# Kernel optimization log

Measured on AMD Instinct MI355X. Metric: run time of the kernel, lower is better.

## Reference

```python
import jax, jax.numpy as jnp
import numpy as np

N_USER = 20000
N_ITEM = 20000
N = N_USER + N_ITEM          # total nodes
D = 128                      # n_hid (= in_feats = out_feats)
H = 4                        # GAT heads
L = 2                        # n_layers
M = 8                        # mem_size (hypernet bottleneck)
T = 5                        # num_rels in MemoryLayer
E_UI = 40000                 # user->item bipartite edges
E_T = 16000                  # homogeneous edges per relation type (grouped)
EPS = 1e-5


def _layer_norm(x, w, b):
    mu = x.mean(-1, keepdims=True)
    var = ((x - mu) ** 2).mean(-1, keepdims=True)
    return (x - mu) * jax.lax.rsqrt(var + EPS) * w + b


def _gat(h_src, h_dst, src_idx, dst_idx, n_dst, W, al, ar, bias):
    """DGL GATConv (shared fc, eval-mode dropout=identity, elu activation)."""
    fs = (h_src @ W.T).reshape(-1, H, D)          # [Ns, H, D]
    fd = (h_dst @ W.T).reshape(-1, H, D)          # [Nd, H, D]
    el = (fs * al).sum(-1)                        # [Ns, H]
    er = (fd * ar).sum(-1)                        # [Nd, H]
    e = jax.nn.leaky_relu(el[src_idx] + er[dst_idx], 0.2)   # [E, H]
    emax = jax.ops.segment_max(e, dst_idx, num_segments=n_dst)
    ex = jnp.exp(e - emax[dst_idx])
    denom = jax.ops.segment_sum(ex, dst_idx, num_segments=n_dst)
    a = ex / denom[dst_idx]                       # edge softmax per dst
    rst = jax.ops.segment_sum(a[:, :, None] * fs[src_idx], dst_idx, num_segments=n_dst)
    return jax.nn.elu(rst + bias.reshape(1, H, D))           # [Nd, H, D]


def _memory_layer(feat, edge_src, edge_dst, Wc, bc, Ww, nWc, nbc, nWw, h_bias, ln_w, ln_b):
    # edges grouped by relation type: edge_src/edge_dst are [T, E_T]
    hs = feat[edge_src]                           # [T, Et, D]
    hd = feat[edge_dst]                           # [T, Et, D]
    # per-edge hypernetwork: coef = LeakyReLU(Linear(dst)); w = Ww(coef); msg = w @ src
    coef = jax.nn.leaky_relu(jnp.einsum('ted,tmd->tem', hd, Wc) + bc[:, None, :], 0.2)
    tmp = jnp.einsum('tei,tmoi->temo', hs, Ww)    # [T, Et, M, D] -- M-bottleneck path
    msg = jnp.einsum('tem,temo->teo', coef, tmp)  # [T, Et, D]
    flat_dst = edge_dst.reshape(-1)
    s = jax.ops.segment_sum(msg.reshape(-1, D), flat_dst, num_segments=N)
    cnt = jax.ops.segment_sum(jnp.ones((flat_dst.shape[0],), feat.dtype), flat_dst, num_segments=N)
    agg = s / jnp.maximum(cnt, 1.0)[:, None]      # fn.mean (0 for isolated nodes)
    rep = _layer_norm(agg, ln_w, ln_b) + h_bias
    # self-loop node_ME(feat, feat)
    ncoef = jax.nn.leaky_relu(feat @ nWc.T + nbc, 0.2)       # [N, M]
    ntmp = jnp.einsum('ni,moi->nmo', feat, nWw)              # [N, M, D]
    rep = rep + jnp.einsum('nm,nmo->no', ncoef, ntmp)
    return jax.nn.leaky_relu(rep, 0.2)            # dropout = identity (eval)


def setup_inputs() -> dict:
    key = jax.random.key(0)
    ks = jax.random.split(key, 16)
    s = 0.05
    return {
        "embedding": jax.random.normal(ks[0], (N, D), jnp.float32),
        "gat_fc_W": jax.random.normal(ks[1], (L, 2, H * D, D), jnp.float32) * s,
        "gat_attn_l": jax.random.normal(ks[2], (L, 2, H, D), jnp.float32) * s,
        "gat_attn_r": jax.random.normal(ks[3], (L, 2, H, D), jnp.float32) * s,
        "gat_bias": jnp.zeros((L, 2, H * D), jnp.float32),
        "proj_W": jax.random.normal(ks[4], (L, 2, D, H * D), jnp.float32) * s,
        "proj_b": jnp.zeros((L, 2, D), jnp.float32),
        "mem_rel_Wc": jax.random.normal(ks[5], (L, T, M, D), jnp.float32) * s,
        "mem_rel_bc": jnp.zeros((L, T, M), jnp.float32),
        "mem_rel_Ww": jax.random.normal(ks[6], (L, T, M, D, D), jnp.float32) * s,
        "mem_node_Wc": jax.random.normal(ks[7], (L, M, D), jnp.float32) * s,
        "mem_node_bc": jnp.zeros((L, M), jnp.float32),
        "mem_node_Ww": jax.random.normal(ks[8], (L, M, D, D), jnp.float32) * s,
        "mem_h_bias": jnp.zeros((L, D), jnp.float32),
        "mem_ln_w": jnp.ones((L, D), jnp.float32),
        "mem_ln_b": jnp.zeros((L, D), jnp.float32),
        "final_ln_w": jnp.ones(((L + 1) * D,), jnp.float32),
        "final_ln_b": jnp.zeros(((L + 1) * D,), jnp.float32),
        "src_u": jax.random.randint(ks[9], (E_UI,), 0, N_USER, jnp.int32),
        "dst_i": jax.random.randint(ks[10], (E_UI,), 0, N_ITEM, jnp.int32),
        "edge_src": jax.random.randint(ks[11], (T, E_T), 0, N, jnp.int32),
        "edge_dst": jax.random.randint(ks[12], (T, E_T), 0, N, jnp.int32),
    }


def reference(embedding, gat_fc_W, gat_attn_l, gat_attn_r, gat_bias, proj_W, proj_b,
              mem_rel_Wc, mem_rel_bc, mem_rel_Ww, mem_node_Wc, mem_node_bc, mem_node_Ww,
              mem_h_bias, mem_ln_w, mem_ln_b, final_ln_w, final_ln_b,
              src_u, dst_i, edge_src, edge_dst):
    features = embedding
    all_emb = [features]
    for l in range(L):
        hu, hi = features[:N_USER], features[N_USER:]
        # relation 0: item -> user (dst = user)
        gu = _gat(hi, hu, dst_i, src_u, N_USER,
                  gat_fc_W[l, 0], gat_attn_l[l, 0], gat_attn_r[l, 0], gat_bias[l, 0])
        ru = jax.nn.elu(gu.reshape(N_USER, H * D) @ proj_W[l, 0].T + proj_b[l, 0])
        # relation 1: user -> item (dst = item)
        gi = _gat(hu, hi, src_u, dst_i, N_ITEM,
                  gat_fc_W[l, 1], gat_attn_l[l, 1], gat_attn_r[l, 1], gat_bias[l, 1])
        ri = jnp.asarray(jax.nn.elu(gi.reshape(N_ITEM, H * D) @ proj_W[l, 1].T + proj_b[l, 1]))
        trans = jnp.concatenate([ru, ri], axis=0)             # [N, D]
        mem = _memory_layer(all_emb[-1], edge_src, edge_dst,
                            mem_rel_Wc[l], mem_rel_bc[l], mem_rel_Ww[l],
                            mem_node_Wc[l], mem_node_bc[l], mem_node_Ww[l],
                            mem_h_bias[l], mem_ln_w[l], mem_ln_b[l])
        features = mem + trans
        all_emb.append(features)
    return _layer_norm(jnp.concatenate(all_emb, axis=1), final_ln_w, final_ln_b)
```

## Files before the change

### kernel.cpp

```cpp
#include <hip/hip_runtime.h>
#include <hip/hip_bf16.h>
#include <math.h>

typedef __hip_bfloat16 bf16;

#define NUSER 20000
#define NITEM 20000
#define NTOT  40000
#define DD    128
#define HH    4
#define TT    5
#define MMEM  8
#define EUI   40000
#define ET    16000

#define MP_N  40064
#define MP_H  20096

typedef __attribute__((ext_vector_type(8))) short short8;
typedef __attribute__((ext_vector_type(4))) float f32x4;

__device__ __forceinline__ void gload16(const bf16* g, bf16* l){
  __builtin_amdgcn_global_load_lds(
      (const __attribute__((address_space(1))) unsigned int*)g,
      (__attribute__((address_space(3))) unsigned int*)l, 16, 0, 0);
}
__device__ __forceinline__ float bu2f_lo(unsigned u){ return __uint_as_float(u << 16); }
__device__ __forceinline__ float bu2f_hi(unsigned u){ return __uint_as_float(u & 0xffff0000u); }

__device__ __forceinline__ int stage_cg(int lane){
  return (((lane&3) ^ ((lane>>2)&3) ^ (lane>>4)) << 3);
}
__device__ __forceinline__ int read_pc8(int lm, int lq){
  return ((lq ^ (lm&3) ^ ((lm>>2)&3)) << 3);
}

__global__ __launch_bounds__(256) void k_mfma_gemm(
    const bf16* __restrict__ A, const bf16* __restrict__ B,
    const float* __restrict__ bias, float* __restrict__ C,
    long Astr, long Bstr, long biasStr, long Cstr,
    int ldc, int M, int K, int act, int accum)
{
  A += (size_t)blockIdx.z*Astr; B += (size_t)blockIdx.z*Bstr;
  if (bias) bias += (size_t)blockIdx.z*biasStr;
  C += (size_t)blockIdx.z*Cstr;
  __shared__ bf16 As[128*32];
  __shared__ bf16 Bs[128*32];
  int tid = threadIdx.x;
  int wave = tid >> 6, lane = tid & 63;
  int r0 = blockIdx.x * 128, c0 = blockIdx.y * 128;
  int wm = (wave >> 1) * 64, wn = (wave & 1) * 64;
  f32x4 acc[4][4];
  #pragma unroll
  for (int i=0;i<4;i++)
    #pragma unroll
    for (int j=0;j<4;j++) acc[i][j] = (f32x4){0.f,0.f,0.f,0.f};

  int rq = lane >> 2;
  int cg = stage_cg(lane);
  const bf16* Ag = A + (size_t)(r0 + wave*32 + rq)*K + cg;
  const bf16* Bg = B + (size_t)(c0 + wave*32 + rq)*K + cg;
  bf16* AsW = As + wave*32*32;
  bf16* BsW = Bs + wave*32*32;
  int lm = lane & 15, lq = lane >> 4;
  int pc8 = read_pc8(lm, lq);
  const bf16* Ard = As + (wm + lm)*32 + pc8;
  const bf16* Brd = Bs + (wn + lm)*32 + pc8;

  for (int k0 = 0; k0 < K; k0 += 32){
    gload16(Ag + k0,            AsW);
    gload16(Ag + 16*K + k0,     AsW + 16*32);
    gload16(Bg + k0,            BsW);
    gload16(Bg + 16*K + k0,     BsW + 16*32);
    __syncthreads();
    short8 af[4], bfv[4];
    #pragma unroll
    for (int i=0;i<4;i++) af[i]  = *(const short8*)(Ard + i*16*32);
    #pragma unroll
    for (int j=0;j<4;j++) bfv[j] = *(const short8*)(Brd + j*16*32);
    #pragma unroll
    for (int i=0;i<4;i++)
      #pragma unroll
      for (int j=0;j<4;j++)
        acc[i][j] = __builtin_amdgcn_mfma_f32_16x16x32_bf16(af[i], bfv[j], acc[i][j], 0, 0, 0);
    __syncthreads();
  }
  #pragma unroll
  for (int i=0;i<4;i++){
    #pragma unroll
    for (int j=0;j<4;j++){
      int c = c0 + wn + j*16 + lm;
      #pragma unroll
      for (int rg=0; rg<4; rg++){
        int r = r0 + wm + i*16 + lq*4 + rg;
        if (r < M){
          float v = acc[i][j][rg];
          if (bias) v += bias[c];
          if (act==1) v = v>0.f ? v : expm1f(v);
          float* cp = &C[(size_t)r*ldc + c];
          if (accum) *cp += v; else *cp = v;
        }
      }
    }
  }
}

__global__ __launch_bounds__(256) void k_fc_gemm(
    const bf16* __restrict__ A, const bf16* __restrict__ B,
    bf16* __restrict__ Fb, const float* __restrict__ al, const float* __restrict__ ar,
    float* __restrict__ el, float* __restrict__ er, int M)
{
  __shared__ bf16 As[128*32];
  __shared__ bf16 Bs[128*32];
  __shared__ float redE[2][2][128];
  int tid = threadIdx.x;
  int wave = tid >> 6, lane = tid & 63;
  int h = blockIdx.y;
  int r0 = blockIdx.x * 128;
  int wm = (wave >> 1) * 64, wn = (wave & 1) * 64;
  f32x4 acc[4][4];
  #pragma unroll
  for (int i=0;i<4;i++)
    #pragma unroll
    for (int j=0;j<4;j++) acc[i][j] = (f32x4){0.f,0.f,0.f,0.f};

  int rq = lane >> 2;
  int cg = stage_cg(lane);
  const bf16* Ag = A + (size_t)(r0 + wave*32 + rq)*128 + cg;
  const bf16* Bg = B + (size_t)(h*128 + wave*32 + rq)*128 + cg;
  bf16* AsW = As + wave*32*32;
  bf16* BsW = Bs + wave*32*32;
  int lm = lane & 15, lq = lane >> 4;
  int pc8 = read_pc8(lm, lq);
  const bf16* Ard = As + (wm + lm)*32 + pc8;
  const bf16* Brd = Bs + (wn + lm)*32 + pc8;

  for (int k0 = 0; k0 < 128; k0 += 32){
    gload16(Ag + k0,             AsW);
    gload16(Ag + 16*128 + k0,    AsW + 16*32);
    gload16(Bg + k0,             BsW);
    gload16(Bg + 16*128 + k0,    BsW + 16*32);
    __syncthreads();
    short8 af[4], bfv[4];
    #pragma unroll
    for (int i=0;i<4;i++) af[i]  = *(const short8*)(Ard + i*16*32);
    #pragma unroll
    for (int j=0;j<4;j++) bfv[j] = *(const short8*)(Brd + j*16*32);
    #pragma unroll
    for (int i=0;i<4;i++)
      #pragma unroll
      for (int j=0;j<4;j++)
        acc[i][j] = __builtin_amdgcn_mfma_f32_16x16x32_bf16(af[i], bfv[j], acc[i][j], 0, 0, 0);
    __syncthreads();
  }
  float alv[4], arv[4];
  #pragma unroll
  for (int j=0;j<4;j++){
    int c = h*128 + wn + j*16 + lm;
    alv[j] = al[c]; arv[j] = ar[c];
  }
  int wnh = wave & 1;
  #pragma unroll
  for (int i=0;i<4;i++){
    #pragma unroll
    for (int rg=0; rg<4; rg++){
      float se = 0.f, sr = 0.f;
      #pragma unroll
      for (int j=0;j<4;j++){
        float v = acc[i][j][rg];
        se = fmaf(v, alv[j], se);
        sr = fmaf(v, arv[j], sr);
      }
      #pragma unroll
      for (int msk=1; msk<16; msk<<=1){
        se += __shfl_xor(se, msk);
        sr += __shfl_xor(sr, msk);
      }
      if (lm == 0){
        int rl = wm + i*16 + lq*4 + rg;
        redE[0][wnh][rl] = se;
        redE[1][wnh][rl] = sr;
      }
    }
  }
  #pragma unroll
  for (int i=0;i<4;i++){
    #pragma unroll
    for (int j=0;j<4;j++){
      int c = h*128 + wn + j*16 + lm;
      #pragma unroll
      for (int rg=0; rg<4; rg++){
        int r = r0 + wm + i*16 + lq*4 + rg;
        if (r < M) Fb[(size_t)r*512 + c] = __float2bfloat16(acc[i][j][rg]);
      }
    }
  }
  __syncthreads();
  if (tid < 128){
    int r = r0 + tid;
    if (r < M) el[(size_t)r*4 + h] = redE[0][0][tid] + redE[0][1][tid];
  } else {
    int t2 = tid - 128;
    int r = r0 + t2;
    if (r < M) er[(size_t)r*4 + h] = redE[1][0][t2] + redE[1][1][t2];
  }
}

__global__ __launch_bounds__(256) void k_memgemm(
    const float* __restrict__ feat, const int* __restrict__ src,
    const float* __restrict__ coef, const bf16* __restrict__ B,
    float* __restrict__ C, bf16* __restrict__ Cb,
    const float* __restrict__ trans, float* __restrict__ fout,
    long srcStr, long coefStr, long Bstr, long CbStr,
    int Mvalid, int mode)
{
  __shared__ bf16 Af[64*136];
  __shared__ float cfS[8*64];
  int t = blockIdx.y;
  const int*   srcT  = src ? src + (size_t)t*srcStr : nullptr;
  const float* coefT = coef + (size_t)t*coefStr;
  const bf16*  Bt    = B + (size_t)t*Bstr;
  int tid = threadIdx.x, wave = tid >> 6, lane = tid & 63;
  int r0 = blockIdx.x * 64;

  {
    int rL = tid >> 2, seg = tid & 3;
    int r = r0 + rL;
    bool valid = r < Mvalid;
    int s = valid ? (srcT ? srcT[r] : r) : 0;
    const float4* fp = (const float4*)(feat + (size_t)s*128 + seg*32);
    bf16* ap = Af + rL*136 + seg*32;
    #pragma unroll
    for (int q=0;q<8;q+=2){
      float4 v0 = fp[q], v1 = fp[q+1];
      *(__hip_bfloat162*)(ap + q*4)     = __float22bfloat162_rn(make_float2(v0.x, v0.y));
      *(__hip_bfloat162*)(ap + q*4 + 2) = __float22bfloat162_rn(make_float2(v0.z, v0.w));
      *(__hip_bfloat162*)(ap + q*4 + 4) = __float22bfloat162_rn(make_float2(v1.x, v1.y));
      *(__hip_bfloat162*)(ap + q*4 + 6) = __float22bfloat162_rn(make_float2(v1.z, v1.w));
    }
  }
  if (tid < 64){
    int r = r0 + tid;
    bool valid = r < Mvalid;
    #pragma unroll
    for (int m=0;m<8;m++)
      cfS[m*64 + tid] = valid ? coefT[(size_t)r*8 + m] : 0.f;
  }
  __syncthreads();

  int wm = (wave >> 1) * 32, wn = (wave & 1) * 64;
  int lm = lane & 15, lq = lane >> 4;

  short8 afr[4][2];
  #pragma unroll
  for (int ic=0; ic<4; ic++)
    #pragma unroll
    for (int i=0; i<2; i++)
      afr[ic][i] = *(const short8*)(Af + (size_t)(wm + i*16 + lm)*136 + ic*32 + lq*8);

  const bf16* Bl0 = Bt + (size_t)(wn +  0 + lm)*1024 + lq*8;
  const bf16* Bl1 = Bt + (size_t)(wn + 16 + lm)*1024 + lq*8;
  const bf16* Bl2 = Bt + (size_t)(wn + 32 + lm)*1024 + lq*8;
  const bf16* Bl3 = Bt + (size_t)(wn + 48 + lm)*1024 + lq*8;

  f32x4 accC[2][4];
  #pragma unroll
  for (int i=0;i<2;i++)
    #pragma unroll
    for (int j=0;j<4;j++) accC[i][j] = (f32x4){0.f,0.f,0.f,0.f};

  #pragma unroll
  for (int m = 0; m < 8; m++){
    f32x4 accM[2][4];
    #pragma unroll
    for (int ic = 0; ic < 4; ic++){
      int ko = m*128 + ic*32;
      short8 bfv[4];
      bfv[0] = *(const short8*)(Bl0 + ko);
      bfv[1] = *(const short8*)(Bl1 + ko);
      bfv[2] = *(const short8*)(Bl2 + ko);
      bfv[3] = *(const short8*)(Bl3 + ko);
      if (ic == 0){
        #pragma unroll
        for (int i=0;i<2;i++)
          #pragma unroll
          for (int j=0;j<4;j++)
            accM[i][j] = __builtin_amdgcn_mfma_f32_16x16x32_bf16(afr[ic][i], bfv[j],
                             (f32x4){0.f,0.f,0.f,0.f}, 0, 0, 0);
      } else {
        #pragma unroll
        for (int i=0;i<2;i++)
          #pragma unroll
          for (int j=0;j<4;j++)
            accM[i][j] = __builtin_amdgcn_mfma_f32_16x16x32_bf16(afr[ic][i], bfv[j], accM[i][j], 0, 0, 0);
      }
    }
    #pragma unroll
    for (int i=0;i<2;i++){
      f32x4 cf4 = *(const f32x4*)(cfS + m*64 + wm + i*16 + lq*4);
      #pragma unroll
      for (int j=0;j<4;j++)
        #pragma unroll
        for (int rg=0; rg<4; rg++)
          accC[i][j][rg] = fmaf(cf4[rg], accM[i][j][rg], accC[i][j][rg]);
    }
  }

  #pragma unroll
  for (int i=0;i<2;i++){
    #pragma unroll
    for (int j=0;j<4;j++){
      int c = wn + j*16 + lm;
      #pragma unroll
      for (int rg=0; rg<4; rg++){
        int r = r0 + wm + i*16 + lq*4 + rg;
        if (r < Mvalid){
          float v = accC[i][j][rg];
          if (mode == 0){
            Cb[(size_t)t*CbStr + (size_t)r*128 + c] = __float2bfloat16(v);
          } else {
            float x = C[(size_t)r*128 + c] + v;
            x = x>0.f ? x : 0.2f*x;
            fout[(size_t)r*128 + c] = x + trans[(size_t)r*128 + c];
          }
        }
      }
    }
  }
}

__global__ void k_f2b(const float* __restrict__ in, bf16* __restrict__ o, int nv, int nt){
  int i = blockIdx.x*256 + threadIdx.x;
  if (i < nt) o[i] = __float2bfloat16(i < nv ? in[i] : 0.f);
}

__global__ void k_repack(const float* __restrict__ in, bf16* __restrict__ o){
  int s = blockIdx.y;
  int g = blockIdx.x*256 + threadIdx.x;
  int m = g >> 14, od = (g >> 7) & 127, i = g & 127;
  o[(size_t)s*131072 + (size_t)od*1024 + m*128 + i] = __float2bfloat16(in[(size_t)s*131072 + g]);
}

__global__ void k_hist(const int* __restrict__ dIdx, int* __restrict__ cnt, int E){
  int e = blockIdx.x*256+threadIdx.x;
  if (e<E) atomicAdd(&cnt[dIdx[e]], 1);
}

__global__ __launch_bounds__(1024) void k_scan(const int* __restrict__ in,
                                               int* __restrict__ out, int n){
  __shared__ int wsum[16];
  __shared__ int carry;
  int tidx = threadIdx.x, lane = tidx & 63, w = tidx >> 6;
  if (tidx == 0) carry = 0;
  __syncthreads();
  for (int base = 0; base < n; base += 1024){
    int i = base + tidx;
    int v = (i < n) ? in[i] : 0;
    int x = v;
    #pragma unroll
    for (int off = 1; off < 64; off <<= 1){
      int t = __shfl_up(x, off);
      if (lane >= off) x += t;
    }
    if (lane == 63) wsum[w] = x;
    __syncthreads();
    if (w == 0 && lane < 16){
      int t = wsum[lane];
      #pragma unroll
      for (int off=1; off<16; off<<=1){
        int u = __shfl_up(t, off, 16);
        if (lane >= off) t += u;
      }
      wsum[lane] = t;
    }
    __syncthreads();
    int woff = (w == 0) ? 0 : wsum[w-1];
    int excl = carry + woff + x - v;
    if (i < n) out[i] = excl;
    __syncthreads();
    if (tidx == 1023) carry = carry + wsum[15];
    __syncthreads();
  }
  if (tidx == 0) out[n] = carry;
}

__global__ void k_csr_scatter(const int* __restrict__ sIdx, const int* __restrict__ dIdx,
                              int sOff, const int* __restrict__ rowptr,
                              int* __restrict__ cursor, int* __restrict__ col, int E){
  int e = blockIdx.x*256+threadIdx.x; if (e>=E) return;
  int d = dIdx[e];
  int pos = rowptr[d] + atomicAdd(&cursor[d], 1);
  col[pos] = sIdx[e] + sOff;
}

__global__ void k_csr_scatter_eid(const int* __restrict__ dIdx, const int* __restrict__ rowptr,
                                  int* __restrict__ cursor, int* __restrict__ col, int E){
  int e = blockIdx.x*256+threadIdx.x; if (e>=E) return;
  int d = dIdx[e];
  int pos = rowptr[d] + atomicAdd(&cursor[d], 1);
  col[pos] = e;
}

__global__ __launch_bounds__(64) void k_gat_gather(
    const int* __restrict__ rowptr, const int* __restrict__ col,
    const float* __restrict__ el, const float* __restrict__ er,
    const bf16* __restrict__ Fb, const float* __restrict__ gb,
    bf16* __restrict__ rstb, int dOff)
{
  int dl = blockIdx.x;
  int lane = threadIdx.x;
  int h = lane >> 4;
  int off = (lane & 15) << 3;
  float erh = er[(size_t)(dl + dOff)*4 + h];
  float m = -INFINITY, den = 0.f;
  float acc[8];
  #pragma unroll
  for (int i=0;i<8;i++) acc[i]=0.f;
  int jb = rowptr[dl], je = rowptr[dl+1];
  for (int j=jb; j<je; j++){
    int s = col[j];
    float e = el[(size_t)s*4+h] + erh;
    e = e > 0.f ? e : 0.2f*e;
    float mn = fmaxf(m, e);
    float sc = __expf(m - mn);
    float wj = __expf(e - mn);
    den = den*sc + wj;
    m = mn;
    uint4 u = *(const uint4*)(Fb + (size_t)s*512 + h*128 + off);
    acc[0]=acc[0]*sc + wj*bu2f_lo(u.x); acc[1]=acc[1]*sc + wj*bu2f_hi(u.x);
    acc[2]=acc[2]*sc + wj*bu2f_lo(u.y); acc[3]=acc[3]*sc + wj*bu2f_hi(u.y);
    acc[4]=acc[4]*sc + wj*bu2f_lo(u.z); acc[5]=acc[5]*sc + wj*bu2f_hi(u.z);
    acc[6]=acc[6]*sc + wj*bu2f_lo(u.w); acc[7]=acc[7]*sc + wj*bu2f_hi(u.w);
  }
  float inv = den > 0.f ? 1.f/den : 0.f;
  int cb = h*128 + off;
  float x[8];
  #pragma unroll
  for (int q=0;q<8;q++){
    float v = acc[q]*inv + gb[cb+q];
    x[q] = v>0.f ? v : expm1f(v);
  }
  union { uint4 u; __hip_bfloat162 p[4]; } O;
  #pragma unroll
  for (int q=0;q<4;q++) O.p[q] = __float22bfloat162_rn(make_float2(x[2*q], x[2*q+1]));
  *(uint4*)(rstb + (size_t)dl*512 + cb) = O.u;
}

__global__ void k_coef(const float* __restrict__ feat, const int* __restrict__ idx,
                       const float* __restrict__ Wc, const float* __restrict__ bc,
                       float* __restrict__ outc, int cnt){
  int t = blockIdx.y;
  __shared__ float wT[DD*MMEM];
  __shared__ float bS[MMEM];
  for (int i=threadIdx.x;i<MMEM*DD;i+=128){
    int m = i >> 7, d = i & 127;
    wT[d*MMEM + m] = Wc[(size_t)t*MMEM*DD + i];
  }
  if (threadIdx.x < MMEM) bS[threadIdx.x] = bc[t*MMEM + threadIdx.x];
  __syncthreads();
  int e = blockIdx.x*128 + threadIdx.x; if (e >= cnt) return;
  int node = idx ? idx[(size_t)t*cnt + e] : e;
  float acc[MMEM];
  #pragma unroll
  for (int m=0;m<MMEM;m++) acc[m]=bS[m];
  const float4* fr = (const float4*)(feat + (size_t)node*DD);
  for (int d4=0; d4<32; d4++){
    float4 v = fr[d4];
    const float* w0 = wT + d4*4*MMEM;
    #pragma unroll
    for (int m=0;m<MMEM;m++) acc[m] = fmaf(v.x, w0[m], acc[m]);
    #pragma unroll
    for (int m=0;m<MMEM;m++) acc[m] = fmaf(v.y, w0[MMEM+m], acc[m]);
    #pragma unroll
    for (int m=0;m<MMEM;m++) acc[m] = fmaf(v.z, w0[2*MMEM+m], acc[m]);
    #pragma unroll
    for (int m=0;m<MMEM;m++) acc[m] = fmaf(v.w, w0[3*MMEM+m], acc[m]);
  }
  float* op = outc + ((size_t)t*cnt + e)*MMEM;
  #pragma unroll
  for (int m=0;m<MMEM;m++){ float v=acc[m]; op[m] = v>0.f ? v : 0.2f*v; }
}

__global__ void k_mem_gather(const int* __restrict__ rpT, const int* __restrict__ colT,
                             const bf16* __restrict__ msg, float* __restrict__ sAgg){
  int n = blockIdx.x*4 + (threadIdx.x >> 6);
  if (n >= NTOT) return;
  int lane = threadIdx.x & 63;
  int jb = rpT[n], je = rpT[n+1];
  float a0=0.f, a1=0.f;
  for (int j=jb;j<je;j++){
    unsigned u = ((const unsigned*)(msg + (size_t)colT[j]*128))[lane];
    a0 += bu2f_lo(u); a1 += bu2f_hi(u);
  }
  *(float2*)(sAgg + (size_t)n*128 + lane*2) = make_float2(a0, a1);
}

__global__ void k_memln(const float* __restrict__ s, const int* __restrict__ rpT,
                        const float* __restrict__ lw, const float* __restrict__ lb,
                        const float* __restrict__ hb, float* __restrict__ outp){
  int n = blockIdx.x, lane = threadIdx.x;
  float c = fmaxf((float)(rpT[n+1]-rpT[n]), 1.f);
  float x1 = s[(size_t)n*128+lane]/c, x2 = s[(size_t)n*128+64+lane]/c;
  float t = x1+x2;
  #pragma unroll
  for (int off=32;off;off>>=1) t += __shfl_xor(t,off);
  float mu = t * (1.f/128.f);
  float d1=x1-mu, d2=x2-mu;
  float v = d1*d1+d2*d2;
  #pragma unroll
  for (int off=32;off;off>>=1) v += __shfl_xor(v,off);
  float r = rsqrtf(v*(1.f/128.f) + 1e-5f);
  outp[(size_t)n*128+lane]    = d1*r*lw[lane]    + lb[lane]    + hb[lane];
  outp[(size_t)n*128+64+lane] = d2*r*lw[64+lane] + lb[64+lane] + hb[64+lane];
}

__global__ void k_final_ln(const float* __restrict__ emb, const float* __restrict__ f1,
                           const float* __restrict__ f2, const float* __restrict__ w,
                           const float* __restrict__ b, float* __restrict__ out){
  int n = blockIdx.x, t = threadIdx.x;
  __shared__ float red[4];
  float x0 = emb[(size_t)n*128+t];
  float x1 = f1[(size_t)n*128+t];
  float x2 = f2[(size_t)n*128+t];
  float s = x0+x1+x2;
  #pragma unroll
  for (int off=32;off;off>>=1) s += __shfl_xor(s,off);
  if ((t&63)==0) red[t>>6] = s;
  __syncthreads();
  float mu = (red[0]+red[1]) * (1.f/384.f);
  float d0=x0-mu, d1=x1-mu, d2=x2-mu;
  float v = d0*d0+d1*d1+d2*d2;
  #pragma unroll
  for (int off=32;off;off>>=1) v += __shfl_xor(v,off);
  if ((t&63)==0) red[2+(t>>6)] = v;
  __syncthreads();
  float var = (red[2]+red[3]) * (1.f/384.f);
  float r = rsqrtf(var + 1e-5f);
  size_t o = (size_t)n*384;
  out[o+t]     = d0*r*w[t]     + b[t];
  out[o+128+t] = d1*r*w[128+t] + b[128+t];
  out[o+256+t] = d2*r*w[256+t] + b[256+t];
}

extern "C" void kernel_launch(void* const* d_in, const int* in_sizes, int n_in,
                              void* d_out, int out_size, void* d_ws, size_t ws_size,
                              hipStream_t stream)
{
  const float* emb   = (const float*)d_in[0];
  const float* fcW   = (const float*)d_in[1];
  const float* attl  = (const float*)d_in[2];
  const float* attr  = (const float*)d_in[3];
  const float* gbias = (const float*)d_in[4];
  const float* projW = (const float*)d_in[5];
  const float* projB = (const float*)d_in[6];
  const float* relWc = (const float*)d_in[7];
  const float* relbc = (const float*)d_in[8];
  const float* relWw = (const float*)d_in[9];
  const float* nodWc = (const float*)d_in[10];
  const float* nodbc = (const float*)d_in[11];
  const float* nodWw = (const float*)d_in[12];
  const float* hbias = (const float*)d_in[13];
  const float* mlnw  = (const float*)d_in[14];
  const float* mlnb  = (const float*)d_in[15];
  const float* flnw  = (const float*)d_in[16];
  const float* flnb  = (const float*)d_in[17];
  const int*  srcU  = (const int*)d_in[18];
  const int*  dstI  = (const int*)d_in[19];
  const int*  eSrc  = (const int*)d_in[20];
  const int*  eDst  = (const int*)d_in[21];
  float* out = (float*)d_out;

  char* wp = (char*)d_ws;
  auto alloc = [&](size_t bytes)->void* {
    void* p = (void*)wp; wp += (bytes + 511) & ~(size_t)511; return p;
  };
  float* feat1 = (float*)alloc((size_t)NTOT*DD*4);
  float* feat2 = (float*)alloc((size_t)NTOT*DD*4);
  float* Fbuf  = (float*)alloc((size_t)NTOT*512*4);
  float* rst   = (float*)alloc((size_t)NTOT*DD*2*4);
  bf16*  rstb0 = (bf16*)alloc((size_t)2*MP_H*512*2);
  float* trans = (float*)alloc((size_t)NTOT*DD*4);
  float* elF   = (float*)alloc((size_t)NTOT*4*4);
  float* erF   = (float*)alloc((size_t)NTOT*4*4);
  int* rpA  = (int*)alloc((size_t)(NUSER+1)*4);
  int* colA = (int*)alloc((size_t)EUI*4);
  int* rpB  = (int*)alloc((size_t)(NITEM+1)*4);
  int* colB = (int*)alloc((size_t)EUI*4);
  int* icnt = (int*)alloc((size_t)20000*4);
  int* icur = (int*)alloc((size_t)20000*4);
  int* rpT  = (int*)alloc((size_t)(NTOT+1)*4);
  int* colT = (int*)alloc((size_t)TT*ET*4);
  int* cntT = (int*)alloc((size_t)NTOT*4);
  int* icurT= (int*)alloc((size_t)NTOT*4);
  bf16* featb  = (bf16*)alloc((size_t)MP_N*DD*2);
  bf16* fcWb   = (bf16*)alloc((size_t)4*512*DD*2);
  bf16* projWb = (bf16*)alloc((size_t)4*DD*512*2);
  bf16* relWwb = (bf16*)alloc((size_t)10*DD*1024*2);
  bf16* nodWwb = (bf16*)alloc((size_t)2*DD*1024*2);
  bf16*  Fb     = (bf16*)Fbuf;
  bf16*  msgBb  = (bf16*)((char*)Fbuf + (size_t)NTOT*512*2);
  float* coefB  = (float*)((char*)msgBb + (size_t)TT*ET*128*2);
  float* ncoefB = coefB + (size_t)TT*ET*8;
  bf16*  rstb1  = rstb0 + (size_t)MP_H*512;
  float* sAgg   = rst;
  float* memO   = rst + (size_t)NTOT*DD;

  k_f2b<<<dim3((4*512*DD+255)/256),256,0,stream>>>(fcW, fcWb, 4*512*DD, 4*512*DD);
  k_f2b<<<dim3((4*DD*512+255)/256),256,0,stream>>>(projW, projWb, 4*DD*512, 4*DD*512);
  k_repack<<<dim3(512,10),256,0,stream>>>(relWw, relWwb);
  k_repack<<<dim3(512,2),256,0,stream>>>(nodWw, nodWwb);
  hipMemsetAsync(rstb0 + (size_t)20000*512, 0, (size_t)(MP_H-20000)*512*2, stream);
  hipMemsetAsync(rstb1 + (size_t)20000*512, 0, (size_t)(MP_H-20000)*512*2, stream);

  hipMemsetAsync(icnt, 0, 20000*4, stream);
  hipMemsetAsync(icur, 0, 20000*4, stream);
  k_hist<<<dim3((EUI+255)/256),256,0,stream>>>(srcU, icnt, EUI);
  k_scan<<<dim3(1),1024,0,stream>>>(icnt, rpA, NUSER);
  k_csr_scatter<<<dim3((EUI+255)/256),256,0,stream>>>(dstI, srcU, NUSER, rpA, icur, colA, EUI);
  hipMemsetAsync(icnt, 0, 20000*4, stream);
  hipMemsetAsync(icur, 0, 20000*4, stream);
  k_hist<<<dim3((EUI+255)/256),256,0,stream>>>(dstI, icnt, EUI);
  k_scan<<<dim3(1),1024,0,stream>>>(icnt, rpB, NITEM);
  k_csr_scatter<<<dim3((EUI+255)/256),256,0,stream>>>(srcU, dstI, 0, rpB, icur, colB, EUI);
  hipMemsetAsync(cntT, 0, NTOT*4, stream);
  hipMemsetAsync(icurT, 0, NTOT*4, stream);
  k_hist<<<dim3((TT*ET+255)/256),256,0,stream>>>(eDst, cntT, TT*ET);
  k_scan<<<dim3(1),1024,0,stream>>>(cntT, rpT, NTOT);
  k_csr_scatter_eid<<<dim3((TT*ET+255)/256),256,0,stream>>>(eDst, rpT, icurT, colT, TT*ET);

  const float* feats[3] = {emb, feat1, feat2};
  for (int l=0; l<2; l++){
    const float* fin  = feats[l];
    float* fout = (float*)feats[l+1];

    k_f2b<<<dim3((MP_N*DD+255)/256),256,0,stream>>>(fin, featb, NTOT*DD, MP_N*DD);

    for (int d=0; d<2; d++){
      k_fc_gemm<<<dim3(MP_N/128, 4),256,0,stream>>>(
          featb, fcWb + (size_t)(l*2+d)*512*DD, Fb,
          attl+(size_t)(l*2+d)*512, attr+(size_t)(l*2+d)*512, elF, erF, NTOT);
      int dOff = (d==0) ? 0 : NUSER;
      const int* rp  = (d==0) ? rpA : rpB;
      const int* col = (d==0) ? colA : colB;
      k_gat_gather<<<dim3(20000),64,0,stream>>>(rp, col, elF, erF, Fb,
          gbias+(size_t)(l*2+d)*512, (d==0) ? rstb0 : rstb1, dOff);
    }
    k_mfma_gemm<<<dim3(MP_H/128, 1, 2),256,0,stream>>>(
        rstb0, projWb + (size_t)(l*2)*DD*512, projB + (size_t)(l*2)*DD, trans,
        (long)MP_H*512, (long)DD*512, (long)DD, (long)20000*DD,
        DD, 20000, 512, 1, 0);

    k_coef<<<dim3((ET+127)/128, TT),128,0,stream>>>(fin, eDst,
        relWc+(size_t)l*TT*MMEM*DD, relbc+(size_t)l*TT*MMEM, coefB, ET);
    k_memgemm<<<dim3(ET/64, TT),256,0,stream>>>(
        fin, eSrc, coefB, relWwb + (size_t)l*TT*DD*1024,
        nullptr, msgBb, nullptr, nullptr,
        (long)ET, (long)ET*8, (long)DD*1024, (long)ET*128, ET, 0);
    k_mem_gather<<<dim3(NTOT/4),256,0,stream>>>(rpT, colT, msgBb, sAgg);
    k_memln<<<dim3(NTOT),64,0,stream>>>(sAgg, rpT, mlnw+(size_t)l*DD, mlnb+(size_t)l*DD,
                                        hbias+(size_t)l*DD, memO);
    k_coef<<<dim3((NTOT+127)/128, 1),128,0,stream>>>(fin, nullptr,
        nodWc+(size_t)l*MMEM*DD, nodbc+(size_t)l*MMEM, ncoefB, NTOT);
    k_memgemm<<<dim3(MP_N/64, 1),256,0,stream>>>(
        fin, nullptr, ncoefB, nodWwb + (size_t)l*DD*1024,
        memO, nullptr, trans, fout,
        0, 0, 0, 0, NTOT, 2);
  }

  k_final_ln<<<dim3(NTOT),128,0,stream>>>(emb, feat1, feat2, flnw, flnb, out);
}
```

Before: 1.021 ms.

## Retile memgemm B weights into k-chunks and double-buffer B loads

Repacks the hypernetwork weight matrix so that each 32-wide k-chunk for all 128 output columns is contiguous, which gives compact, coalesced B fragment loads. The memgemm inner loop now prefetches the next chunk's B fragments into a second register set while the MFMAs for the current chunk run. It also adds a minimum occupancy of 3 blocks per CU to launch_bounds. The aim is to hide global load latency for B. The extra register buffer, combined with the occupancy target, could lead to spills.

New measurement: 1.805 ms. 1.77x slower.

```diff
diff --git a/kernel.cpp b/kernel.cpp
--- a/kernel.cpp
+++ b/kernel.cpp
@@ -206,7 +206,7 @@
   }
 }
 
-__global__ __launch_bounds__(256) void k_memgemm(
+__global__ __launch_bounds__(256,3) void k_memgemm(
     const float* __restrict__ feat, const int* __restrict__ src,
     const float* __restrict__ coef, const bf16* __restrict__ B,
     float* __restrict__ C, bf16* __restrict__ Cb,
@@ -258,10 +258,33 @@
     for (int i=0; i<2; i++)
       afr[ic][i] = *(const short8*)(Af + (size_t)(wm + i*16 + lm)*136 + ic*32 + lq*8);
 
-  const bf16* Bl0 = Bt + (size_t)(wn +  0 + lm)*1024 + lq*8;
-  const bf16* Bl1 = Bt + (size_t)(wn + 16 + lm)*1024 + lq*8;
-  const bf16* Bl2 = Bt + (size_t)(wn + 32 + lm)*1024 + lq*8;
-  const bf16* Bl3 = Bt + (size_t)(wn + 48 + lm)*1024 + lq*8;
+  const bf16* Bl = Bt + (size_t)(wn + lm)*32 + lq*8;
+
+#define LDB(dst, kc) do{                                    \
+    const bf16* _p = Bl + (size_t)(kc)*4096;                \
+    dst[0] = *(const short8*)(_p);                          \
+    dst[1] = *(const short8*)(_p + 512);                    \
+    dst[2] = *(const short8*)(_p + 1024);                   \
+    dst[3] = *(const short8*)(_p + 1536);                   \
+  }while(0)
+
+#define MFMA_STEP(ic, bv) do{                                                        \
+    if ((ic)==0){                                                                    \
+      _Pragma("unroll")                                                              \
+      for (int i=0;i<2;i++)                                                          \
+        _Pragma("unroll")                                                            \
+        for (int j=0;j<4;j++)                                                        \
+          accM[i][j] = __builtin_amdgcn_mfma_f32_16x16x32_bf16(afr[0][i], bv[j],     \
+                           (f32x4){0.f,0.f,0.f,0.f}, 0, 0, 0);                       \
+    } else {                                                                         \
+      _Pragma("unroll")                                                              \
+      for (int i=0;i<2;i++)                                                          \
+        _Pragma("unroll")                                                            \
+        for (int j=0;j<4;j++)                                                        \
+          accM[i][j] = __builtin_amdgcn_mfma_f32_16x16x32_bf16(afr[ic][i], bv[j],    \
+                           accM[i][j], 0, 0, 0);                                     \
+    }                                                                                \
+  }while(0)
 
   f32x4 accC[2][4];
   #pragma unroll
@@ -269,30 +292,21 @@
     #pragma unroll
     for (int j=0;j<4;j++) accC[i][j] = (f32x4){0.f,0.f,0.f,0.f};
 
+  short8 bcur[4], bnxt[4];
+  LDB(bcur, 0);
+  f32x4 accM[2][4];
+
   #pragma unroll
   for (int m = 0; m < 8; m++){
-    f32x4 accM[2][4];
     #pragma unroll
     for (int ic = 0; ic < 4; ic++){
-      int ko = m*128 + ic*32;
-      short8 bfv[4];
-      bfv[0] = *(const short8*)(Bl0 + ko);
-      bfv[1] = *(const short8*)(Bl1 + ko);
-      bfv[2] = *(const short8*)(Bl2 + ko);
-      bfv[3] = *(const short8*)(Bl3 + ko);
-      if (ic == 0){
-        #pragma unroll
-        for (int i=0;i<2;i++)
-          #pragma unroll
-          for (int j=0;j<4;j++)
-            accM[i][j] = __builtin_amdgcn_mfma_f32_16x16x32_bf16(afr[ic][i], bfv[j],
-                             (f32x4){0.f,0.f,0.f,0.f}, 0, 0, 0);
+      const int kc = m*4 + ic;
+      if ((kc & 1) == 0){
+        if (kc + 1 < 32) LDB(bnxt, kc+1);
+        MFMA_STEP(ic, bcur);
       } else {
-        #pragma unroll
-        for (int i=0;i<2;i++)
-          #pragma unroll
-          for (int j=0;j<4;j++)
-            accM[i][j] = __builtin_amdgcn_mfma_f32_16x16x32_bf16(afr[ic][i], bfv[j], accM[i][j], 0, 0, 0);
+        if (kc + 1 < 32) LDB(bcur, kc+1);
+        MFMA_STEP(ic, bnxt);
       }
     }
     #pragma unroll
@@ -305,6 +319,8 @@
           accC[i][j][rg] = fmaf(cf4[rg], accM[i][j][rg], accC[i][j][rg]);
     }
   }
+#undef LDB
+#undef MFMA_STEP
 
   #pragma unroll
   for (int i=0;i<2;i++){
@@ -338,7 +354,9 @@
   int s = blockIdx.y;
   int g = blockIdx.x*256 + threadIdx.x;
   int m = g >> 14, od = (g >> 7) & 127, i = g & 127;
-  o[(size_t)s*131072 + (size_t)od*1024 + m*128 + i] = __float2bfloat16(in[(size_t)s*131072 + g]);
+  int k = m*128 + i;
+  int kc = k >> 5, ki = k & 31;
+  o[(size_t)s*131072 + ((size_t)kc*128 + od)*32 + ki] = __float2bfloat16(in[(size_t)s*131072 + g]);
 }
 
 __global__ void k_hist(const int* __restrict__ dIdx, int* __restrict__ cnt, int E){
```

## Fold hypernet coefficients into a K=1024 A matrix and reuse the generic MFMA GEMM

Applied to the files above, without the earlier changes.

Replaces the fused memory-layer kernel, which ran eight K=128 MFMA passes per tile and scaled each by per-row coefficients, with two steps. A new kernel first writes a bf16 A matrix of coef[m]*feat rows (K=1024), and the shared LDS-staged MFMA GEMM then multiplies it by the repacked Ww weights. The GEMM epilogue gains bf16 output and a fused leaky-relu plus trans-add mode. This aims for a better-pipelined, LDS-tiled GEMM at the cost of materialising a large intermediate (about 165MB for the relation path), plus a fallback that runs per relation or per half when the workspace is too small.

Result: slower. 1.338 ms (+31.0%).

```diff
diff --git a/kernel.cpp b/kernel.cpp
--- a/kernel.cpp
+++ b/kernel.cpp
@@ -16,6 +16,7 @@
 
 #define MP_N  40064
 #define MP_H  20096
+#define EP_PAD 16128
 
 typedef __attribute__((ext_vector_type(8))) short short8;
 typedef __attribute__((ext_vector_type(4))) float f32x4;
@@ -37,13 +38,14 @@
 
 __global__ __launch_bounds__(256) void k_mfma_gemm(
     const bf16* __restrict__ A, const bf16* __restrict__ B,
-    const float* __restrict__ bias, float* __restrict__ C,
-    long Astr, long Bstr, long biasStr, long Cstr,
-    int ldc, int M, int K, int act, int accum)
+    const float* __restrict__ bias,
+    float* __restrict__ C, bf16* __restrict__ Cb,
+    const float* __restrict__ Cin, const float* __restrict__ trans,
+    long Astr, long Bstr, long biasStr, long Cstr, long CbStr,
+    int ldc, int M, int K, int act)
 {
   A += (size_t)blockIdx.z*Astr; B += (size_t)blockIdx.z*Bstr;
   if (bias) bias += (size_t)blockIdx.z*biasStr;
-  C += (size_t)blockIdx.z*Cstr;
   __shared__ bf16 As[128*32];
   __shared__ bf16 Bs[128*32];
   int tid = threadIdx.x;
@@ -97,8 +99,13 @@
           float v = acc[i][j][rg];
           if (bias) v += bias[c];
           if (act==1) v = v>0.f ? v : expm1f(v);
-          float* cp = &C[(size_t)r*ldc + c];
-          if (accum) *cp += v; else *cp = v;
+          if (act==2){
+            float x = Cin[(size_t)r*128 + c] + v;
+            x = x>0.f ? x : 0.2f*x;
+            v = x + trans[(size_t)r*128 + c];
+          }
+          if (Cb) Cb[(size_t)blockIdx.z*CbStr + (size_t)r*ldc + c] = __float2bfloat16(v);
+          else    C [(size_t)blockIdx.z*Cstr  + (size_t)r*ldc + c] = v;
         }
       }
     }
@@ -206,127 +213,31 @@
   }
 }
 
-__global__ __launch_bounds__(256) void k_memgemm(
-    const float* __restrict__ feat, const int* __restrict__ src,
-    const float* __restrict__ coef, const bf16* __restrict__ B,
-    float* __restrict__ C, bf16* __restrict__ Cb,
-    const float* __restrict__ trans, float* __restrict__ fout,
-    long srcStr, long coefStr, long Bstr, long CbStr,
-    int Mvalid, int mode)
+__global__ void k_bldA(const float* __restrict__ feat, const int* __restrict__ src,
+                       const float* __restrict__ cf, bf16* __restrict__ out,
+                       int rows, int rowsPad, int rowOff,
+                       long srcStr, long cfStr, long outStr)
 {
-  __shared__ bf16 Af[64*136];
-  __shared__ float cfS[8*64];
   int t = blockIdx.y;
-  const int*   srcT  = src ? src + (size_t)t*srcStr : nullptr;
-  const float* coefT = coef + (size_t)t*coefStr;
-  const bf16*  Bt    = B + (size_t)t*Bstr;
-  int tid = threadIdx.x, wave = tid >> 6, lane = tid & 63;
-  int r0 = blockIdx.x * 64;
-
-  {
-    int rL = tid >> 2, seg = tid & 3;
-    int r = r0 + rL;
-    bool valid = r < Mvalid;
-    int s = valid ? (srcT ? srcT[r] : r) : 0;
-    const float4* fp = (const float4*)(feat + (size_t)s*128 + seg*32);
-    bf16* ap = Af + rL*136 + seg*32;
-    #pragma unroll
-    for (int q=0;q<8;q+=2){
-      float4 v0 = fp[q], v1 = fp[q+1];
-      *(__hip_bfloat162*)(ap + q*4)     = __float22bfloat162_rn(make_float2(v0.x, v0.y));
-      *(__hip_bfloat162*)(ap + q*4 + 2) = __float22bfloat162_rn(make_float2(v0.z, v0.w));
-      *(__hip_bfloat162*)(ap + q*4 + 4) = __float22bfloat162_rn(make_float2(v1.x, v1.y));
-      *(__hip_bfloat162*)(ap + q*4 + 6) = __float22bfloat162_rn(make_float2(v1.z, v1.w));
-    }
-  }
-  if (tid < 64){
-    int r = r0 + tid;
-    bool valid = r < Mvalid;
-    #pragma unroll
-    for (int m=0;m<8;m++)
-      cfS[m*64 + tid] = valid ? coefT[(size_t)r*8 + m] : 0.f;
-  }
-  __syncthreads();
-
-  int wm = (wave >> 1) * 32, wn = (wave & 1) * 64;
-  int lm = lane & 15, lq = lane >> 4;
-
-  short8 afr[4][2];
-  #pragma unroll
-  for (int ic=0; ic<4; ic++)
-    #pragma unroll
-    for (int i=0; i<2; i++)
-      afr[ic][i] = *(const short8*)(Af + (size_t)(wm + i*16 + lm)*136 + ic*32 + lq*8);
-
-  const bf16* Bl0 = Bt + (size_t)(wn +  0 + lm)*1024 + lq*8;
-  const bf16* Bl1 = Bt + (size_t)(wn + 16 + lm)*1024 + lq*8;
-  const bf16* Bl2 = Bt + (size_t)(wn + 32 + lm)*1024 + lq*8;
-  const bf16* Bl3 = Bt + (size_t)(wn + 48 + lm)*1024 + lq*8;
-
-  f32x4 accC[2][4];
-  #pragma unroll
-  for (int i=0;i<2;i++)
-    #pragma unroll
-    for (int j=0;j<4;j++) accC[i][j] = (f32x4){0.f,0.f,0.f,0.f};
-
-  #pragma unroll
-  for (int m = 0; m < 8; m++){
-    f32x4 accM[2][4];
-    #pragma unroll
-    for (int ic = 0; ic < 4; ic++){
-      int ko = m*128 + ic*32;
-      short8 bfv[4];
-      bfv[0] = *(const short8*)(Bl0 + ko);
-      bfv[1] = *(const short8*)(Bl1 + ko);
-      bfv[2] = *(const short8*)(Bl2 + ko);
-      bfv[3] = *(const short8*)(Bl3 + ko);
-      if (ic == 0){
-        #pragma unroll
-        for (int i=0;i<2;i++)
-          #pragma unroll
-          for (int j=0;j<4;j++)
-            accM[i][j] = __builtin_amdgcn_mfma_f32_16x16x32_bf16(afr[ic][i], bfv[j],
-                             (f32x4){0.f,0.f,0.f,0.f}, 0, 0, 0);
-      } else {
-        #pragma unroll
-        for (int i=0;i<2;i++)
-          #pragma unroll
-          for (int j=0;j<4;j++)
-            accM[i][j] = __builtin_amdgcn_mfma_f32_16x16x32_bf16(afr[ic][i], bfv[j], accM[i][j], 0, 0, 0);
-      }
-    }
-    #pragma unroll
-    for (int i=0;i<2;i++){
-      f32x4 cf4 = *(const f32x4*)(cfS + m*64 + wm + i*16 + lq*4);
-      #pragma unroll
-      for (int j=0;j<4;j++)
-        #pragma unroll
-        for (int rg=0; rg<4; rg++)
-          accC[i][j][rg] = fmaf(cf4[rg], accM[i][j][rg], accC[i][j][rg]);
-    }
-  }
-
-  #pragma unroll
-  for (int i=0;i<2;i++){
-    #pragma unroll
-    for (int j=0;j<4;j++){
-      int c = wn + j*16 + lm;
-      #pragma unroll
-      for (int rg=0; rg<4; rg++){
-        int r = r0 + wm + i*16 + lq*4 + rg;
-        if (r < Mvalid){
-          float v = accC[i][j][rg];
-          if (mode == 0){
-            Cb[(size_t)t*CbStr + (size_t)r*128 + c] = __float2bfloat16(v);
-          } else {
-            float x = C[(size_t)r*128 + c] + v;
-            x = x>0.f ? x : 0.2f*x;
-            fout[(size_t)r*128 + c] = x + trans[(size_t)r*128 + c];
-          }
-        }
-      }
-    }
-  }
+  long g = (long)blockIdx.x*256 + threadIdx.x;
+  long row = g >> 7;
+  if (row >= rowsPad) return;
+  int grp = (int)(g & 127);
+  int k0 = grp*8, m = k0 >> 7, i0 = k0 & 127;
+  bool valid = row < rows;
+  int s = 0; float c = 0.f;
+  if (valid){
+    s = src ? src[(size_t)t*srcStr + row] : (int)(rowOff + row);
+    c = cf[((size_t)t*cfStr + rowOff + row)*8 + m];
+  }
+  const float4* fp = (const float4*)(feat + (size_t)s*128 + i0);
+  float4 v0 = fp[0], v1 = fp[1];
+  union { uint4 u; __hip_bfloat162 p[4]; } O;
+  O.p[0] = __float22bfloat162_rn(make_float2(c*v0.x, c*v0.y));
+  O.p[1] = __float22bfloat162_rn(make_float2(c*v0.z, c*v0.w));
+  O.p[2] = __float22bfloat162_rn(make_float2(c*v1.x, c*v1.y));
+  O.p[3] = __float22bfloat162_rn(make_float2(c*v1.z, c*v1.w));
+  *(uint4*)(out + (size_t)t*outStr + (size_t)row*1024 + k0) = O.u;
 }
 
 __global__ void k_f2b(const float* __restrict__ in, bf16* __restrict__ o, int nv, int nt){
@@ -605,6 +516,12 @@
   float* sAgg   = rst;
   float* memO   = rst + (size_t)NTOT*DD;
 
+  size_t used0 = (size_t)(wp - (char*)d_ws);
+  size_t ABIG  = (size_t)TT*EP_PAD*1024*2;
+  bool bigA = (ws_size >= used0 + ABIG);
+  bf16* Abig = bigA ? (bf16*)alloc(ABIG) : nullptr;
+  bf16* Asm  = (bf16*)Fbuf;
+
   k_f2b<<<dim3((4*512*DD+255)/256),256,0,stream>>>(fcW, fcWb, 4*512*DD, 4*512*DD);
   k_f2b<<<dim3((4*DD*512+255)/256),256,0,stream>>>(projW, projWb, 4*DD*512, 4*DD*512);
   k_repack<<<dim3(512,10),256,0,stream>>>(relWw, relWwb);
@@ -646,25 +563,56 @@
           gbias+(size_t)(l*2+d)*512, (d==0) ? rstb0 : rstb1, dOff);
     }
     k_mfma_gemm<<<dim3(MP_H/128, 1, 2),256,0,stream>>>(
-        rstb0, projWb + (size_t)(l*2)*DD*512, projB + (size_t)(l*2)*DD, trans,
-        (long)MP_H*512, (long)DD*512, (long)DD, (long)20000*DD,
-        DD, 20000, 512, 1, 0);
+        rstb0, projWb + (size_t)(l*2)*DD*512, projB + (size_t)(l*2)*DD,
+        trans, nullptr, nullptr, nullptr,
+        (long)MP_H*512, (long)DD*512, (long)DD, (long)20000*DD, 0,
+        DD, 20000, 512, 1);
 
     k_coef<<<dim3((ET+127)/128, TT),128,0,stream>>>(fin, eDst,
         relWc+(size_t)l*TT*MMEM*DD, relbc+(size_t)l*TT*MMEM, coefB, ET);
-    k_memgemm<<<dim3(ET/64, TT),256,0,stream>>>(
-        fin, eSrc, coefB, relWwb + (size_t)l*TT*DD*1024,
-        nullptr, msgBb, nullptr, nullptr,
-        (long)ET, (long)ET*8, (long)DD*1024, (long)ET*128, ET, 0);
+    if (bigA){
+      k_bldA<<<dim3(EP_PAD>>1, TT),256,0,stream>>>(fin, eSrc, coefB, Abig,
+          ET, EP_PAD, 0, (long)ET, (long)ET, (long)EP_PAD*1024);
+      k_mfma_gemm<<<dim3(EP_PAD/128, 1, TT),256,0,stream>>>(
+          Abig, relWwb + (size_t)l*TT*131072, nullptr,
+          nullptr, msgBb, nullptr, nullptr,
+          (long)EP_PAD*1024, 131072, 0, 0, (long)ET*128,
+          128, ET, 1024, 0);
+    } else {
+      for (int t=0; t<TT; t++){
+        k_bldA<<<dim3(EP_PAD>>1, 1),256,0,stream>>>(fin, eSrc+(size_t)t*ET,
+            coefB+(size_t)t*ET*8, Asm, ET, EP_PAD, 0, 0, 0, 0);
+        k_mfma_gemm<<<dim3(EP_PAD/128, 1, 1),256,0,stream>>>(
+            Asm, relWwb + (size_t)(l*TT+t)*131072, nullptr,
+            nullptr, msgBb + (size_t)t*ET*128, nullptr, nullptr,
+            0, 0, 0, 0, 0, 128, ET, 1024, 0);
+      }
+    }
     k_mem_gather<<<dim3(NTOT/4),256,0,stream>>>(rpT, colT, msgBb, sAgg);
     k_memln<<<dim3(NTOT),64,0,stream>>>(sAgg, rpT, mlnw+(size_t)l*DD, mlnb+(size_t)l*DD,
                                         hbias+(size_t)l*DD, memO);
     k_coef<<<dim3((NTOT+127)/128, 1),128,0,stream>>>(fin, nullptr,
         nodWc+(size_t)l*MMEM*DD, nodbc+(size_t)l*MMEM, ncoefB, NTOT);
-    k_memgemm<<<dim3(MP_N/64, 1),256,0,stream>>>(
-        fin, nullptr, ncoefB, nodWwb + (size_t)l*DD*1024,
-        memO, nullptr, trans, fout,
-        0, 0, 0, 0, NTOT, 2);
+    if (bigA){
+      k_bldA<<<dim3(MP_N>>1, 1),256,0,stream>>>(fin, nullptr, ncoefB, Abig,
+          NTOT, MP_N, 0, 0, 0, 0);
+      k_mfma_gemm<<<dim3(MP_N/128, 1, 1),256,0,stream>>>(
+          Abig, nodWwb + (size_t)l*131072, nullptr,
+          fout, nullptr, memO, trans,
+          0, 0, 0, 0, 0, 128, NTOT, 1024, 2);
+    } else {
+      for (int h=0; h<2; h++){
+        int off = h*MP_H;
+        int cnt = (h==0) ? MP_H : (NTOT - MP_H);
+        k_bldA<<<dim3(MP_H>>1, 1),256,0,stream>>>(fin, nullptr, ncoefB, Asm,
+            cnt, MP_H, off, 0, 0, 0);
+        k_mfma_gemm<<<dim3(MP_H/128, 1, 1),256,0,stream>>>(
+            Asm, nodWwb + (size_t)l*131072, nullptr,
+            fout + (size_t)off*128, nullptr,
+            memO + (size_t)off*128, trans + (size_t)off*128,
+            0, 0, 0, 0, 0, 128, cnt, 1024, 2);
+      }
+    }
   }
 
   k_final_ln<<<dim3(NTOT),128,0,stream>>>(emb, feat1, feat2, flnw, flnb, out);
```

## Triple-buffer LDS tiles with async global-to-LDS loads in GEMM kernels

Applied to the files above, without the earlier changes.

Both the generic MFMA GEMM and the memory-layer hypernet GEMM now use a three-stage LDS ring filled by global_load_lds, with explicit vmcnt waits and a single barrier per k-step. This replaces the double-sync load-then-compute loop and, in the memory GEMM, direct per-lane global loads of B. The aim is to overlap global-memory latency with MFMA work. The cost is more LDS per block, which can lower occupancy, and fragile hand-written waitcnt counts.

Result: faster. 913.8 us (-10.5%).

```diff
diff --git a/kernel.cpp b/kernel.cpp
--- a/kernel.cpp
+++ b/kernel.cpp
@@ -44,8 +44,8 @@
   A += (size_t)blockIdx.z*Astr; B += (size_t)blockIdx.z*Bstr;
   if (bias) bias += (size_t)blockIdx.z*biasStr;
   C += (size_t)blockIdx.z*Cstr;
-  __shared__ bf16 As[128*32];
-  __shared__ bf16 Bs[128*32];
+  __shared__ bf16 As[3][4096];
+  __shared__ bf16 Bs[3][4096];
   int tid = threadIdx.x;
   int wave = tid >> 6, lane = tid & 63;
   int r0 = blockIdx.x * 128, c0 = blockIdx.y * 128;
@@ -60,30 +60,52 @@
   int cg = stage_cg(lane);
   const bf16* Ag = A + (size_t)(r0 + wave*32 + rq)*K + cg;
   const bf16* Bg = B + (size_t)(c0 + wave*32 + rq)*K + cg;
-  bf16* AsW = As + wave*32*32;
-  bf16* BsW = Bs + wave*32*32;
   int lm = lane & 15, lq = lane >> 4;
   int pc8 = read_pc8(lm, lq);
-  const bf16* Ard = As + (wm + lm)*32 + pc8;
-  const bf16* Brd = Bs + (wn + lm)*32 + pc8;
-
-  for (int k0 = 0; k0 < K; k0 += 32){
-    gload16(Ag + k0,            AsW);
-    gload16(Ag + 16*K + k0,     AsW + 16*32);
-    gload16(Bg + k0,            BsW);
-    gload16(Bg + 16*K + k0,     BsW + 16*32);
-    __syncthreads();
+
+  int ns = K >> 5;
+  {
+    bf16* dA = &As[0][wave*1024]; bf16* dB = &Bs[0][wave*1024];
+    gload16(Ag,        dA); gload16(Ag + 16*K, dA + 512);
+    gload16(Bg,        dB); gload16(Bg + 16*K, dB + 512);
+  }
+  if (ns > 1){
+    bf16* dA = &As[1][wave*1024]; bf16* dB = &Bs[1][wave*1024];
+    gload16(Ag + 32,        dA); gload16(Ag + 16*K + 32, dA + 512);
+    gload16(Bg + 32,        dB); gload16(Bg + 16*K + 32, dB + 512);
+    asm volatile("s_waitcnt vmcnt(4)" ::: "memory");
+  } else {
+    asm volatile("s_waitcnt vmcnt(0)" ::: "memory");
+  }
+  __builtin_amdgcn_s_barrier();
+
+  int cur = 0, stg = 2;
+  for (int i = 0; i < ns; i++){
+    if (i + 2 < ns){
+      int k2 = (i + 2) << 5;
+      bf16* dA = &As[stg][wave*1024]; bf16* dB = &Bs[stg][wave*1024];
+      gload16(Ag + k2,        dA); gload16(Ag + 16*K + k2, dA + 512);
+      gload16(Bg + k2,        dB); gload16(Bg + 16*K + k2, dB + 512);
+    }
+    const bf16* Ard = &As[cur][(wm + lm)*32 + pc8];
+    const bf16* Brd = &Bs[cur][(wn + lm)*32 + pc8];
     short8 af[4], bfv[4];
     #pragma unroll
-    for (int i=0;i<4;i++) af[i]  = *(const short8*)(Ard + i*16*32);
-    #pragma unroll
-    for (int j=0;j<4;j++) bfv[j] = *(const short8*)(Brd + j*16*32);
-    #pragma unroll
-    for (int i=0;i<4;i++)
+    for (int ii=0;ii<4;ii++) af[ii]  = *(const short8*)(Ard + ii*16*32);
+    #pragma unroll
+    for (int j=0;j<4;j++)    bfv[j]  = *(const short8*)(Brd + j*16*32);
+    #pragma unroll
+    for (int ii=0;ii<4;ii++)
       #pragma unroll
       for (int j=0;j<4;j++)
-        acc[i][j] = __builtin_amdgcn_mfma_f32_16x16x32_bf16(af[i], bfv[j], acc[i][j], 0, 0, 0);
-    __syncthreads();
+        acc[ii][j] = __builtin_amdgcn_mfma_f32_16x16x32_bf16(af[ii], bfv[j], acc[ii][j], 0, 0, 0);
+    if (i < ns - 1){
+      if (i + 2 < ns) asm volatile("s_waitcnt vmcnt(4)" ::: "memory");
+      else            asm volatile("s_waitcnt vmcnt(0)" ::: "memory");
+      __builtin_amdgcn_s_barrier();
+    }
+    cur = (cur == 2) ? 0 : cur + 1;
+    stg = (stg == 2) ? 0 : stg + 1;
   }
   #pragma unroll
   for (int i=0;i<4;i++){
@@ -216,6 +238,7 @@
 {
   __shared__ bf16 Af[64*136];
   __shared__ float cfS[8*64];
+  __shared__ bf16 Bs[3][4096];
   int t = blockIdx.y;
   const int*   srcT  = src ? src + (size_t)t*srcStr : nullptr;
   const float* coefT = coef + (size_t)t*coefStr;
@@ -246,10 +269,23 @@
     for (int m=0;m<8;m++)
       cfS[m*64 + tid] = valid ? coefT[(size_t)r*8 + m] : 0.f;
   }
-  __syncthreads();
-
+
+  int rq = lane >> 2;
+  int cg = stage_cg(lane);
+  const bf16* Bg0 = Bt + (size_t)(wave*32 + rq)*1024 + cg;
+  const bf16* Bg1 = Bt + (size_t)(wave*32 + 16 + rq)*1024 + cg;
   int wm = (wave >> 1) * 32, wn = (wave & 1) * 64;
   int lm = lane & 15, lq = lane >> 4;
+  int pc8 = read_pc8(lm, lq);
+
+  {
+    bf16* d0 = &Bs[0][wave*1024];
+    gload16(Bg0,      d0); gload16(Bg1,      d0 + 512);
+    bf16* d1 = &Bs[1][wave*1024];
+    gload16(Bg0 + 32, d1); gload16(Bg1 + 32, d1 + 512);
+  }
+  asm volatile("s_waitcnt lgkmcnt(0) vmcnt(2)" ::: "memory");
+  __builtin_amdgcn_s_barrier();
 
   short8 afr[4][2];
   #pragma unroll
@@ -258,34 +294,34 @@
     for (int i=0; i<2; i++)
       afr[ic][i] = *(const short8*)(Af + (size_t)(wm + i*16 + lm)*136 + ic*32 + lq*8);
 
-  const bf16* Bl0 = Bt + (size_t)(wn +  0 + lm)*1024 + lq*8;
-  const bf16* Bl1 = Bt + (size_t)(wn + 16 + lm)*1024 + lq*8;
-  const bf16* Bl2 = Bt + (size_t)(wn + 32 + lm)*1024 + lq*8;
-  const bf16* Bl3 = Bt + (size_t)(wn + 48 + lm)*1024 + lq*8;
-
   f32x4 accC[2][4];
   #pragma unroll
   for (int i=0;i<2;i++)
     #pragma unroll
     for (int j=0;j<4;j++) accC[i][j] = (f32x4){0.f,0.f,0.f,0.f};
+  f32x4 accM[2][4];
 
   #pragma unroll
   for (int m = 0; m < 8; m++){
-    f32x4 accM[2][4];
     #pragma unroll
     for (int ic = 0; ic < 4; ic++){
-      int ko = m*128 + ic*32;
+      const int kk = m*4 + ic;
+      if (kk + 2 < 32){
+        bf16* d = &Bs[(kk+2)%3][wave*1024];
+        gload16(Bg0 + (kk+2)*32, d);
+        gload16(Bg1 + (kk+2)*32, d + 512);
+      }
+      const bf16* bb = &Bs[kk%3][0];
       short8 bfv[4];
-      bfv[0] = *(const short8*)(Bl0 + ko);
-      bfv[1] = *(const short8*)(Bl1 + ko);
-      bfv[2] = *(const short8*)(Bl2 + ko);
-      bfv[3] = *(const short8*)(Bl3 + ko);
+      #pragma unroll
+      for (int j=0;j<4;j++)
+        bfv[j] = *(const short8*)(bb + (wn + lm + j*16)*32 + pc8);
       if (ic == 0){
         #pragma unroll
         for (int i=0;i<2;i++)
           #pragma unroll
           for (int j=0;j<4;j++)
-            accM[i][j] = __builtin_amdgcn_mfma_f32_16x16x32_bf16(afr[ic][i], bfv[j],
+            accM[i][j] = __builtin_amdgcn_mfma_f32_16x16x32_bf16(afr[0][i], bfv[j],
                              (f32x4){0.f,0.f,0.f,0.f}, 0, 0, 0);
       } else {
         #pragma unroll
@@ -293,6 +329,11 @@
           #pragma unroll
           for (int j=0;j<4;j++)
             accM[i][j] = __builtin_amdgcn_mfma_f32_16x16x32_bf16(afr[ic][i], bfv[j], accM[i][j], 0, 0, 0);
+      }
+      if (kk < 31){
+        if (kk + 2 < 32) asm volatile("s_waitcnt vmcnt(2)" ::: "memory");
+        else             asm volatile("s_waitcnt vmcnt(0)" ::: "memory");
+        __builtin_amdgcn_s_barrier();
       }
     }
     #pragma unroll
```
